# Optimization experiments

Hardware: AMD Instinct MI355X
Metric: run time of the kernel (lower is better)

The kernel has to match this reference:

```python
import jax, jax.numpy as jnp
import numpy as np

B, T, D, E, F, K = 1, 8192, 1024, 8, 4096, 2
CAP_FACTOR = 1.25
AUX_COEFF = 0.01


def setup_inputs() -> dict:
    key = jax.random.key(0)
    k0, k1, k2, k3, k4 = jax.random.split(key, 5)
    x = jax.random.normal(k0, (B, T, D), dtype=jnp.float32)
    Wr = jax.random.normal(k1, (E, D), dtype=jnp.float32) * 0.01  # router, std=0.01 per init
    s = 0.02
    Wg = jax.random.normal(k2, (E, F, D), dtype=jnp.float32) * s  # gate_proj per expert
    Wu = jax.random.normal(k3, (E, F, D), dtype=jnp.float32) * s  # up_proj per expert
    Wd = jax.random.normal(k4, (E, D, F), dtype=jnp.float32) * s  # down_proj per expert
    return {"x": x, "Wr": Wr, "Wg": Wg, "Wu": Wu, "Wd": Wd}


def reference(x, Wr, Wg, Wu, Wd):
    b, t, d = x.shape
    N = b * t
    capacity = max(int(t * K * CAP_FACTOR / E), 1)  # static, matches compute_capacity
    x_flat = x.reshape(N, d)

    # --- router ---
    logits = x_flat @ Wr.T                              # (N, E)
    probs = jax.nn.softmax(logits, axis=-1)
    topw_raw, topi = jax.lax.top_k(probs, K)            # (N, K)
    topw = topw_raw / (topw_raw.sum(-1, keepdims=True) + 1e-9)

    # --- dispatch order: slot-major (slot 0 over all tokens, then slot 1, ...) ---
    flat_e = topi.T.reshape(-1)                         # (K*N,) expert id per assignment
    flat_w = topw.T.reshape(-1)                         # (K*N,)
    tok = jnp.tile(jnp.arange(N), K)                    # (K*N,) token id per assignment

    oh = jax.nn.one_hot(flat_e, E, dtype=jnp.int32)     # (K*N, E)
    rank = (jnp.cumsum(oh, axis=0) - oh)[jnp.arange(K * N), flat_e]  # arrival rank per expert
    accepted = rank < capacity                          # dispatch_mask (slot-major flat)
    pos = jnp.where(accepted, rank, 0)
    dest = flat_e * capacity + pos                      # slot in flattened capacity buffer
    acc_f = accepted.astype(x.dtype)[:, None]

    # scatter tokens into capacity buffers (dropped tokens add zeros)
    buf = jnp.zeros((E * capacity, d), x.dtype).at[dest].add(x_flat[tok] * acc_f)
    expert_in = buf.reshape(E, capacity, d)

    # --- per-expert SwiGLU FFN (batched grouped GEMM) ---
    gate = jax.nn.silu(jnp.einsum('ecd,efd->ecf', expert_in, Wg))
    up = jnp.einsum('ecd,efd->ecf', expert_in, Wu)
    expert_out = jnp.einsum('ecf,edf->ecd', gate * up, Wd).reshape(E * capacity, d)

    # --- weighted combine back to token positions ---
    contrib = flat_w[:, None] * acc_f * expert_out[dest]
    out_flat = jnp.zeros((N, d), x.dtype).at[tok].add(contrib)
    output = out_flat.reshape(b, t, d)

    # --- load-balance aux loss ---
    counts = jnp.zeros(E, x.dtype).at[flat_e].add(accepted.astype(x.dtype))
    total = jnp.maximum(accepted.sum().astype(x.dtype), 1.0)
    f_i = counts / total
    P_i = probs.mean(0)
    aux_loss = AUX_COEFF * E * jnp.sum(f_i * P_i)
    return output, aux_loss
```

## Files before the change

### kernel.cpp

```cpp
#include <hip/hip_runtime.h>
#include <hip/hip_bf16.h>

#define N_TOK 8192
#define DIM   1024
#define NEXP  8
#define FF    4096
#define CAP   2560
#define NASSIGN (N_TOK * 2)

typedef __bf16 bf16;
typedef __bf16 bf16x8 __attribute__((ext_vector_type(8)));
typedef float  f32x4  __attribute__((ext_vector_type(4)));

__device__ __forceinline__ void gl2lds16(const bf16* g, bf16* l) {
    __builtin_amdgcn_global_load_lds(
        (const __attribute__((address_space(1))) unsigned int*)g,
        (__attribute__((address_space(3))) unsigned int*)l,
        16, 0, 0);
}

__global__ __launch_bounds__(256) void cvt_bf16_kernel(const float* __restrict__ in,
                                                       bf16* __restrict__ out, int n) {
    int stride = gridDim.x * blockDim.x * 8;
    for (int i = (blockIdx.x * blockDim.x + threadIdx.x) * 8; i < n; i += stride) {
        float4 a = *(const float4*)(in + i);
        float4 b = *(const float4*)(in + i + 4);
        bf16x8 o;
        o[0] = (bf16)a.x; o[1] = (bf16)a.y; o[2] = (bf16)a.z; o[3] = (bf16)a.w;
        o[4] = (bf16)b.x; o[5] = (bf16)b.y; o[6] = (bf16)b.z; o[7] = (bf16)b.w;
        *(bf16x8*)(out + i) = o;
    }
}

__global__ __launch_bounds__(256) void router_kernel(const float* __restrict__ x,
                                                     const float* __restrict__ Wr,
                                                     float* __restrict__ probs,
                                                     int* __restrict__ topi,
                                                     float* __restrict__ topw) {
    int wave = threadIdx.x >> 6;
    int lane = threadIdx.x & 63;
    int t = blockIdx.x * 4 + wave;
    const float* xr = x + (size_t)t * DIM;

    double acc[NEXP];
#pragma unroll
    for (int e = 0; e < NEXP; ++e) acc[e] = 0.0;
    for (int i = lane; i < DIM; i += 64) {
        double xv = (double)xr[i];
#pragma unroll
        for (int e = 0; e < NEXP; ++e) acc[e] += xv * (double)Wr[e * DIM + i];
    }
#pragma unroll
    for (int e = 0; e < NEXP; ++e) {
        double v = acc[e];
        for (int off = 32; off > 0; off >>= 1) v += __shfl_down(v, off, 64);
        acc[e] = v;
    }
    if (lane == 0) {
        double mx = acc[0];
        for (int e = 1; e < NEXP; ++e) if (acc[e] > mx) mx = acc[e];
        double p[NEXP], s = 0.0;
        for (int e = 0; e < NEXP; ++e) { p[e] = exp(acc[e] - mx); s += p[e]; }
        float pf[NEXP];
        for (int e = 0; e < NEXP; ++e) { pf[e] = (float)(p[e] / s); probs[t * NEXP + e] = pf[e]; }
        int e1 = 0;
        for (int e = 1; e < NEXP; ++e) if (acc[e] > acc[e1]) e1 = e;
        int e2 = -1;
        for (int e = 0; e < NEXP; ++e) {
            if (e == e1) continue;
            if (e2 < 0 || acc[e] > acc[e2]) e2 = e;
        }
        float w1 = pf[e1], w2 = pf[e2];
        float inv = 1.0f / (w1 + w2 + 1e-9f);
        topi[t * 2 + 0] = e1; topi[t * 2 + 1] = e2;
        topw[t * 2 + 0] = w1 * inv; topw[t * 2 + 1] = w2 * inv;
    }
}

__global__ __launch_bounds__(64) void rank_kernel(const int* __restrict__ topi,
                                                  int* __restrict__ dest,
                                                  int* __restrict__ accf,
                                                  int* __restrict__ counts) {
    int e = blockIdx.x;
    int lane = threadIdx.x;
    const int per = NASSIGN / 64;
    int base = lane * per;
    int cnt = 0;
    for (int i = 0; i < per; ++i) {
        int j = base + i;
        int t = j & (N_TOK - 1), s = j >> 13;
        if (topi[t * 2 + s] == e) cnt++;
    }
    int sum = cnt;
    for (int off = 1; off < 64; off <<= 1) {
        int v = __shfl_up(sum, off, 64);
        if (lane >= off) sum += v;
    }
    int r = sum - cnt;
    int total = __shfl(sum, 63, 64);
    for (int i = 0; i < per; ++i) {
        int j = base + i;
        int t = j & (N_TOK - 1), s = j >> 13;
        if (topi[t * 2 + s] == e) {
            int acc = (r < CAP) ? 1 : 0;
            dest[j] = e * CAP + (acc ? r : 0);
            accf[j] = acc;
            r++;
        }
    }
    if (lane == 63) counts[e] = (total < CAP) ? total : CAP;
}

__global__ __launch_bounds__(256) void gather_kernel(const float* __restrict__ x,
                                                     const int* __restrict__ dest,
                                                     const int* __restrict__ accf,
                                                     bf16* __restrict__ Xe) {
    int j = blockIdx.x;
    if (!accf[j]) return;
    int t = j & (N_TOK - 1);
    int d0 = threadIdx.x * 4;
    float4 v = *(const float4*)(x + (size_t)t * DIM + d0);
    union { bf16 h[4]; uint2 u; } tmp;
    tmp.h[0] = (bf16)v.x; tmp.h[1] = (bf16)v.y; tmp.h[2] = (bf16)v.z; tmp.h[3] = (bf16)v.w;
    *(uint2*)(Xe + (size_t)dest[j] * DIM + d0) = tmp.u;
}

__global__ __launch_bounds__(512, 2) void gateup_kernel(const bf16* __restrict__ Xe,
                                                        const bf16* __restrict__ Wg,
                                                        const bf16* __restrict__ Wu,
                                                        bf16* __restrict__ hbuf) {
    const int e = blockIdx.z;
    const int m0 = blockIdx.x * 256;
    const int n0 = blockIdx.y * 128;
    const int tid = threadIdx.x;
    const int lane = tid & 63;
    const int wave = tid >> 6;
    const int wr = wave >> 1;
    const int wc = wave & 1;
    const int r16 = lane & 15, c16 = lane >> 4;

    __shared__ bf16 As [2][256 * 64];
    __shared__ bf16 Bgs[2][128 * 64];
    __shared__ bf16 Bus[2][128 * 64];

    const int rsub = wave * 8 + (lane >> 3);
    const int csw  = ((lane & 7) ^ (lane >> 3)) * 8;
    const bf16* ga = Xe + (size_t)e * CAP * DIM + (size_t)(m0 + rsub) * DIM + csw;
    const bf16* gg = Wg + (size_t)e * FF * DIM + (size_t)(n0 + rsub) * DIM + csw;
    const bf16* gu = Wu + (size_t)e * FF * DIM + (size_t)(n0 + rsub) * DIM + csw;

    f32x4 accg[4][4] = {};
    f32x4 accu[4][4] = {};

    auto STAGE = [&](int kt) {
        const int b = kt & 1;
        const bf16* a = ga + kt * 64;
#pragma unroll
        for (int i = 0; i < 4; ++i)
            gl2lds16(a + (size_t)i * 64 * DIM, &As[b][(i * 64 + wave * 8) * 64]);
        const bf16* g = gg + kt * 64;
#pragma unroll
        for (int i = 0; i < 2; ++i)
            gl2lds16(g + (size_t)i * 64 * DIM, &Bgs[b][(i * 64 + wave * 8) * 64]);
        const bf16* u = gu + kt * 64;
#pragma unroll
        for (int i = 0; i < 2; ++i)
            gl2lds16(u + (size_t)i * 64 * DIM, &Bus[b][(i * 64 + wave * 8) * 64]);
    };

    STAGE(0);
    STAGE(1);

    for (int kt = 0; kt < DIM / 64; ++kt) {
        if (kt < DIM / 64 - 1) asm volatile("s_waitcnt vmcnt(8)" ::: "memory");
        else                   asm volatile("s_waitcnt vmcnt(0)" ::: "memory");
        __builtin_amdgcn_sched_barrier(0);
        __builtin_amdgcn_s_barrier();
        __builtin_amdgcn_sched_barrier(0);
        const int b = kt & 1;
#pragma unroll
        for (int kk = 0; kk < 2; ++kk) {
            bf16x8 a[4], bg[4], bu[4];
#pragma unroll
            for (int m = 0; m < 4; ++m) {
                int row = wr * 64 + m * 16 + r16;
                int phys = (kk * 4 + c16) ^ (row & 7);
                a[m] = *(const bf16x8*)&As[b][row * 64 + phys * 8];
            }
#pragma unroll
            for (int n = 0; n < 4; ++n) {
                int row = wc * 64 + n * 16 + r16;
                int phys = (kk * 4 + c16) ^ (row & 7);
                bg[n] = *(const bf16x8*)&Bgs[b][row * 64 + phys * 8];
            }
            __builtin_amdgcn_s_setprio(1);
#pragma unroll
            for (int m = 0; m < 4; ++m)
#pragma unroll
                for (int n = 0; n < 4; ++n)
                    accg[m][n] = __builtin_amdgcn_mfma_f32_16x16x32_bf16(a[m], bg[n], accg[m][n], 0, 0, 0);
            __builtin_amdgcn_s_setprio(0);
#pragma unroll
            for (int n = 0; n < 4; ++n) {
                int row = wc * 64 + n * 16 + r16;
                int phys = (kk * 4 + c16) ^ (row & 7);
                bu[n] = *(const bf16x8*)&Bus[b][row * 64 + phys * 8];
            }
            __builtin_amdgcn_s_setprio(1);
#pragma unroll
            for (int m = 0; m < 4; ++m)
#pragma unroll
                for (int n = 0; n < 4; ++n)
                    accu[m][n] = __builtin_amdgcn_mfma_f32_16x16x32_bf16(a[m], bu[n], accu[m][n], 0, 0, 0);
            __builtin_amdgcn_s_setprio(0);
        }
        __builtin_amdgcn_sched_barrier(0);
        __builtin_amdgcn_s_barrier();
        __builtin_amdgcn_sched_barrier(0);
        if (kt + 2 < DIM / 64) STAGE(kt + 2);
    }

    bf16* hp = hbuf + (size_t)e * CAP * FF;
#pragma unroll
    for (int m = 0; m < 4; ++m)
#pragma unroll
        for (int n = 0; n < 4; ++n)
#pragma unroll
            for (int j = 0; j < 4; ++j) {
                float g = accg[m][n][j];
                float u = accu[m][n][j];
                float h = (g / (1.f + __expf(-g))) * u;
                int gr = m0 + wr * 64 + m * 16 + c16 * 4 + j;
                int gc = n0 + wc * 64 + n * 16 + r16;
                hp[(size_t)gr * FF + gc] = (bf16)h;
            }
}

__global__ __launch_bounds__(256, 2) void down_kernel(const bf16* __restrict__ hbuf,
                                                      const bf16* __restrict__ Wd,
                                                      float* __restrict__ eo) {
    const int e = blockIdx.z;
    const int m0 = blockIdx.x * 128;
    const int n0 = blockIdx.y * 128;
    const int tid = threadIdx.x;
    const int lane = tid & 63;
    const int wave = tid >> 6;
    const int wr = wave >> 1;
    const int wc = wave & 1;
    const int r16 = lane & 15, c16 = lane >> 4;

    __shared__ bf16 As[2][128 * 64];
    __shared__ bf16 Bs[2][128 * 64];

    const int rsub = wave * 8 + (lane >> 3);
    const int csw  = ((lane & 7) ^ (lane >> 3)) * 8;
    const bf16* gaA = hbuf + (size_t)e * CAP * FF + (size_t)(m0 + rsub) * FF + csw;
    const bf16* gaB = Wd + (size_t)e * DIM * FF + (size_t)(n0 + rsub) * FF + csw;

    f32x4 acc[4][4] = {};

    auto STAGE = [&](int kt) {
        const int b = kt & 1;
        const bf16* a = gaA + kt * 64;
#pragma unroll
        for (int i = 0; i < 4; ++i)
            gl2lds16(a + (size_t)i * 32 * FF, &As[b][(i * 32 + wave * 8) * 64]);
        const bf16* w = gaB + kt * 64;
#pragma unroll
        for (int i = 0; i < 4; ++i)
            gl2lds16(w + (size_t)i * 32 * FF, &Bs[b][(i * 32 + wave * 8) * 64]);
    };

    STAGE(0);
    STAGE(1);

    for (int kt = 0; kt < FF / 64; ++kt) {
        if (kt < FF / 64 - 1) asm volatile("s_waitcnt vmcnt(8)" ::: "memory");
        else                  asm volatile("s_waitcnt vmcnt(0)" ::: "memory");
        __builtin_amdgcn_sched_barrier(0);
        __builtin_amdgcn_s_barrier();
        __builtin_amdgcn_sched_barrier(0);
        const int b = kt & 1;
#pragma unroll
        for (int kk = 0; kk < 2; ++kk) {
            bf16x8 a[4], w[4];
#pragma unroll
            for (int m = 0; m < 4; ++m) {
                int row = wr * 64 + m * 16 + r16;
                int phys = (kk * 4 + c16) ^ (row & 7);
                a[m] = *(const bf16x8*)&As[b][row * 64 + phys * 8];
            }
#pragma unroll
            for (int n = 0; n < 4; ++n) {
                int row = wc * 64 + n * 16 + r16;
                int phys = (kk * 4 + c16) ^ (row & 7);
                w[n] = *(const bf16x8*)&Bs[b][row * 64 + phys * 8];
            }
            __builtin_amdgcn_s_setprio(1);
#pragma unroll
            for (int m = 0; m < 4; ++m)
#pragma unroll
                for (int n = 0; n < 4; ++n)
                    acc[m][n] = __builtin_amdgcn_mfma_f32_16x16x32_bf16(a[m], w[n], acc[m][n], 0, 0, 0);
            __builtin_amdgcn_s_setprio(0);
        }
        __builtin_amdgcn_sched_barrier(0);
        __builtin_amdgcn_s_barrier();
        __builtin_amdgcn_sched_barrier(0);
        if (kt + 2 < FF / 64) STAGE(kt + 2);
    }

    float* op = eo + (size_t)e * CAP * DIM;
#pragma unroll
    for (int m = 0; m < 4; ++m)
#pragma unroll
        for (int n = 0; n < 4; ++n)
#pragma unroll
            for (int j = 0; j < 4; ++j) {
                int gr = m0 + wr * 64 + m * 16 + c16 * 4 + j;
                int gc = n0 + wc * 64 + n * 16 + r16;
                op[(size_t)gr * DIM + gc] = acc[m][n][j];
            }
}

__global__ __launch_bounds__(256) void combine_kernel(const float* __restrict__ eo,
                                                      const int* __restrict__ dest,
                                                      const int* __restrict__ accf,
                                                      const float* __restrict__ topw,
                                                      float* __restrict__ out) {
    int t = blockIdx.x;
    float w0 = accf[t] ? topw[t * 2 + 0] : 0.f;
    float w1 = accf[N_TOK + t] ? topw[t * 2 + 1] : 0.f;
    const float* r0 = eo + (size_t)dest[t] * DIM;
    const float* r1 = eo + (size_t)dest[N_TOK + t] * DIM;
    int d = threadIdx.x * 4;
    float4 a = *(const float4*)(r0 + d);
    float4 b = *(const float4*)(r1 + d);
    float4 o;
    o.x = w0 * a.x + w1 * b.x;
    o.y = w0 * a.y + w1 * b.y;
    o.z = w0 * a.z + w1 * b.z;
    o.w = w0 * a.w + w1 * b.w;
    *(float4*)(out + (size_t)t * DIM + d) = o;
}

__global__ __launch_bounds__(256) void aux_kernel(const float* __restrict__ probs,
                                                  const int* __restrict__ counts,
                                                  float* __restrict__ out_aux) {
    __shared__ float sm[256][NEXP];
    float loc[NEXP];
#pragma unroll
    for (int e = 0; e < NEXP; ++e) loc[e] = 0.f;
    for (int t = threadIdx.x; t < N_TOK; t += 256)
#pragma unroll
        for (int e = 0; e < NEXP; ++e) loc[e] += probs[t * NEXP + e];
#pragma unroll
    for (int e = 0; e < NEXP; ++e) sm[threadIdx.x][e] = loc[e];
    __syncthreads();
    for (int s = 128; s > 0; s >>= 1) {
        if (threadIdx.x < s)
#pragma unroll
            for (int e = 0; e < NEXP; ++e) sm[threadIdx.x][e] += sm[threadIdx.x + s][e];
        __syncthreads();
    }
    if (threadIdx.x == 0) {
        int tot = 0;
        for (int e = 0; e < NEXP; ++e) tot += counts[e];
        float totf = tot > 0 ? (float)tot : 1.f;
        float aux = 0.f;
        for (int e = 0; e < NEXP; ++e)
            aux += ((float)counts[e] / totf) * (sm[0][e] / (float)N_TOK);
        out_aux[0] = 0.01f * (float)NEXP * aux;
    }
}

extern "C" void kernel_launch(void* const* d_in, const int* in_sizes, int n_in,
                              void* d_out, int out_size, void* d_ws, size_t ws_size,
                              hipStream_t stream) {
    const float* x  = (const float*)d_in[0];
    const float* Wr = (const float*)d_in[1];
    const float* Wg = (const float*)d_in[2];
    const float* Wu = (const float*)d_in[3];
    const float* Wd = (const float*)d_in[4];
    float* out = (float*)d_out;

    char* ws = (char*)d_ws;
    size_t off = 0;
    auto alloc = [&](size_t bytes) -> void* {
        void* p = ws + off;
        off += (bytes + 255) & ~(size_t)255;
        return p;
    };
    const size_t NW = (size_t)NEXP * FF * DIM;
    bf16*  Wg_bf = (bf16*)alloc(NW * sizeof(bf16));
    bf16*  Wu_bf = (bf16*)alloc(NW * sizeof(bf16));
    bf16*  Wd_bf = (bf16*)alloc(NW * sizeof(bf16));
    bf16*  Xe    = (bf16*)alloc((size_t)NEXP * CAP * DIM * sizeof(bf16));
    bf16*  hbuf  = (bf16*)alloc((size_t)NEXP * CAP * FF * sizeof(bf16));
    float* eo    = (float*)alloc((size_t)NEXP * CAP * DIM * sizeof(float));
    float* probs = (float*)alloc((size_t)N_TOK * NEXP * sizeof(float));
    int*   topi  = (int*)alloc((size_t)N_TOK * 2 * sizeof(int));
    float* topw  = (float*)alloc((size_t)N_TOK * 2 * sizeof(float));
    int*   dst   = (int*)alloc((size_t)NASSIGN * sizeof(int));
    int*   accf  = (int*)alloc((size_t)NASSIGN * sizeof(int));
    int*   cnts  = (int*)alloc(NEXP * sizeof(int));

    cvt_bf16_kernel<<<2048, 256, 0, stream>>>(Wg, Wg_bf, (int)NW);
    cvt_bf16_kernel<<<2048, 256, 0, stream>>>(Wu, Wu_bf, (int)NW);
    cvt_bf16_kernel<<<2048, 256, 0, stream>>>(Wd, Wd_bf, (int)NW);
    router_kernel<<<N_TOK / 4, 256, 0, stream>>>(x, Wr, probs, topi, topw);
    rank_kernel<<<NEXP, 64, 0, stream>>>(topi, dst, accf, cnts);
    gather_kernel<<<NASSIGN, 256, 0, stream>>>(x, dst, accf, Xe);
    gateup_kernel<<<dim3(CAP / 256, FF / 128, NEXP), 512, 0, stream>>>(Xe, Wg_bf, Wu_bf, hbuf);
    down_kernel<<<dim3(CAP / 128, DIM / 128, NEXP), 256, 0, stream>>>(hbuf, Wd_bf, eo);
    combine_kernel<<<N_TOK, 256, 0, stream>>>(eo, dst, accf, topw, out);
    aux_kernel<<<1, 256, 0, stream>>>(probs, cnts, out + (size_t)N_TOK * DIM);
}
```

Measured before the change: 912.3 us.

## Share a 256x256 four-phase GEMM core; split-K down projection with bf16 partials

Adds a shared 256x256-tile GEMM core that splits each k-step into four phases of LDS reads and MFMAs separated by barriers. The gate/up kernel now interleaves gate and up rows into one 256-row B tile so both products share the A fragments. The down projection moves to 256x256 tiles with split-K over two halves of FF, and writes its partial sums as bf16, which combine adds together. This aims for more MFMA work per byte loaded and enough blocks to fill the GPU, at the cost of lower precision in the down-projection output and more barriers.

```diff
diff --git a/kernel.cpp b/kernel.cpp
--- a/kernel.cpp
+++ b/kernel.cpp
@@ -10,6 +10,7 @@
 
 typedef __bf16 bf16;
 typedef __bf16 bf16x8 __attribute__((ext_vector_type(8)));
+typedef __bf16 bf16x4v __attribute__((ext_vector_type(4)));
 typedef float  f32x4  __attribute__((ext_vector_type(4)));
 
 __device__ __forceinline__ void gl2lds16(const bf16* g, bf16* l) {
@@ -17,6 +18,97 @@
         (const __attribute__((address_space(1))) unsigned int*)g,
         (__attribute__((address_space(3))) unsigned int*)l,
         16, 0, 0);
+}
+
+template <int NT>
+__device__ __forceinline__ void gemm256_core(
+    const bf16* __restrict__ gA, size_t astep,
+    const bf16* __restrict__ gB, size_t bstep,
+    bf16* As, bf16* Bs, f32x4 acc[8][4], int wave, int lane)
+{
+    const int wm = wave >> 2, wn = wave & 3;
+    const int r16 = lane & 15, c16 = lane >> 4;
+
+    auto STAGE = [&](int kt) {
+        const int b = kt & 1;
+        const bf16* a  = gA + kt * 64;
+        const bf16* bb = gB + kt * 64;
+#pragma unroll
+        for (int g = 0; g < 4; ++g)
+            gl2lds16(a + (size_t)g * astep, &As[b * (256 * 64) + (g * 64 + wave * 8) * 64]);
+#pragma unroll
+        for (int g = 0; g < 4; ++g)
+            gl2lds16(bb + (size_t)g * bstep, &Bs[b * (256 * 64) + (g * 64 + wave * 8) * 64]);
+    };
+
+    STAGE(0);
+    STAGE(1);
+
+    bf16x8 af[4][2], bfr[2][2];
+
+    for (int kt = 0; kt < NT; ++kt) {
+        if (kt < NT - 1) asm volatile("s_waitcnt vmcnt(8)" ::: "memory");
+        else             asm volatile("s_waitcnt vmcnt(0)" ::: "memory");
+        __builtin_amdgcn_sched_barrier(0);
+        __builtin_amdgcn_s_barrier();
+        __builtin_amdgcn_sched_barrier(0);
+        const bf16* Asb = &As[(kt & 1) * (256 * 64)];
+        const bf16* Bsb = &Bs[(kt & 1) * (256 * 64)];
+
+#define DS_A(mh)                                                          \
+        _Pragma("unroll")                                                 \
+        for (int m = 0; m < 4; ++m) {                                     \
+            _Pragma("unroll")                                             \
+            for (int kk = 0; kk < 2; ++kk) {                              \
+                int row = wm * 128 + (mh) * 64 + m * 16 + r16;            \
+                int phys = (kk * 4 + c16) ^ (row & 7);                    \
+                af[m][kk] = *(const bf16x8*)&Asb[row * 64 + phys * 8];    \
+            } }
+#define DS_B(nh)                                                          \
+        _Pragma("unroll")                                                 \
+        for (int n = 0; n < 2; ++n) {                                     \
+            _Pragma("unroll")                                             \
+            for (int kk = 0; kk < 2; ++kk) {                              \
+                int row = wn * 64 + ((nh) * 2 + n) * 16 + r16;            \
+                int phys = (kk * 4 + c16) ^ (row & 7);                    \
+                bfr[n][kk] = *(const bf16x8*)&Bsb[row * 64 + phys * 8];   \
+            } }
+#define PH_IN                                                             \
+        __builtin_amdgcn_sched_barrier(0);                                \
+        __builtin_amdgcn_s_barrier();                                     \
+        asm volatile("s_waitcnt lgkmcnt(0)" ::: "memory");                \
+        __builtin_amdgcn_sched_barrier(0);
+#define PH_MFMA(mh, nh)                                                   \
+        __builtin_amdgcn_s_setprio(1);                                    \
+        _Pragma("unroll")                                                 \
+        for (int m = 0; m < 4; ++m)                                       \
+            _Pragma("unroll")                                             \
+            for (int n = 0; n < 2; ++n)                                   \
+                _Pragma("unroll")                                         \
+                for (int kk = 0; kk < 2; ++kk)                            \
+                    acc[(mh) * 4 + m][(nh) * 2 + n] =                     \
+                        __builtin_amdgcn_mfma_f32_16x16x32_bf16(          \
+                            af[m][kk], bfr[n][kk],                        \
+                            acc[(mh) * 4 + m][(nh) * 2 + n], 0, 0, 0);    \
+        __builtin_amdgcn_s_setprio(0);
+#define PH_OUT                                                            \
+        __builtin_amdgcn_sched_barrier(0);                                \
+        __builtin_amdgcn_s_barrier();                                     \
+        __builtin_amdgcn_sched_barrier(0);
+
+        DS_A(0) DS_B(0) PH_IN PH_MFMA(0, 0) PH_OUT
+        DS_B(1)         PH_IN PH_MFMA(0, 1) PH_OUT
+        DS_A(1) DS_B(0) PH_IN PH_MFMA(1, 0) PH_OUT
+        DS_B(1)         PH_IN PH_MFMA(1, 1) PH_OUT
+
+#undef DS_A
+#undef DS_B
+#undef PH_IN
+#undef PH_MFMA
+#undef PH_OUT
+
+        if (kt + 2 < NT) STAGE(kt + 2);
+    }
 }
 
 __global__ __launch_bounds__(256) void cvt_bf16_kernel(const float* __restrict__ in,
@@ -131,199 +223,76 @@
                                                         bf16* __restrict__ hbuf) {
     const int e = blockIdx.z;
     const int m0 = blockIdx.x * 256;
-    const int n0 = blockIdx.y * 128;
-    const int tid = threadIdx.x;
-    const int lane = tid & 63;
-    const int wave = tid >> 6;
-    const int wr = wave >> 1;
-    const int wc = wave & 1;
+    const int n0f = blockIdx.y * 128;
+    const int tid = threadIdx.x, lane = tid & 63, wave = tid >> 6;
+    const int wm = wave >> 2, wn = wave & 3;
     const int r16 = lane & 15, c16 = lane >> 4;
 
-    __shared__ bf16 As [2][256 * 64];
-    __shared__ bf16 Bgs[2][128 * 64];
-    __shared__ bf16 Bus[2][128 * 64];
+    __shared__ bf16 As[2 * 256 * 64];
+    __shared__ bf16 Bs[2 * 256 * 64];
 
     const int rsub = wave * 8 + (lane >> 3);
     const int csw  = ((lane & 7) ^ (lane >> 3)) * 8;
-    const bf16* ga = Xe + (size_t)e * CAP * DIM + (size_t)(m0 + rsub) * DIM + csw;
-    const bf16* gg = Wg + (size_t)e * FF * DIM + (size_t)(n0 + rsub) * DIM + csw;
-    const bf16* gu = Wu + (size_t)e * FF * DIM + (size_t)(n0 + rsub) * DIM + csw;
-
-    f32x4 accg[4][4] = {};
-    f32x4 accu[4][4] = {};
-
-    auto STAGE = [&](int kt) {
-        const int b = kt & 1;
-        const bf16* a = ga + kt * 64;
-#pragma unroll
-        for (int i = 0; i < 4; ++i)
-            gl2lds16(a + (size_t)i * 64 * DIM, &As[b][(i * 64 + wave * 8) * 64]);
-        const bf16* g = gg + kt * 64;
-#pragma unroll
-        for (int i = 0; i < 2; ++i)
-            gl2lds16(g + (size_t)i * 64 * DIM, &Bgs[b][(i * 64 + wave * 8) * 64]);
-        const bf16* u = gu + kt * 64;
-#pragma unroll
-        for (int i = 0; i < 2; ++i)
-            gl2lds16(u + (size_t)i * 64 * DIM, &Bus[b][(i * 64 + wave * 8) * 64]);
-    };
-
-    STAGE(0);
-    STAGE(1);
-
-    for (int kt = 0; kt < DIM / 64; ++kt) {
-        if (kt < DIM / 64 - 1) asm volatile("s_waitcnt vmcnt(8)" ::: "memory");
-        else                   asm volatile("s_waitcnt vmcnt(0)" ::: "memory");
-        __builtin_amdgcn_sched_barrier(0);
-        __builtin_amdgcn_s_barrier();
-        __builtin_amdgcn_sched_barrier(0);
-        const int b = kt & 1;
-#pragma unroll
-        for (int kk = 0; kk < 2; ++kk) {
-            bf16x8 a[4], bg[4], bu[4];
-#pragma unroll
-            for (int m = 0; m < 4; ++m) {
-                int row = wr * 64 + m * 16 + r16;
-                int phys = (kk * 4 + c16) ^ (row & 7);
-                a[m] = *(const bf16x8*)&As[b][row * 64 + phys * 8];
-            }
-#pragma unroll
-            for (int n = 0; n < 4; ++n) {
-                int row = wc * 64 + n * 16 + r16;
-                int phys = (kk * 4 + c16) ^ (row & 7);
-                bg[n] = *(const bf16x8*)&Bgs[b][row * 64 + phys * 8];
-            }
-            __builtin_amdgcn_s_setprio(1);
-#pragma unroll
-            for (int m = 0; m < 4; ++m)
-#pragma unroll
-                for (int n = 0; n < 4; ++n)
-                    accg[m][n] = __builtin_amdgcn_mfma_f32_16x16x32_bf16(a[m], bg[n], accg[m][n], 0, 0, 0);
-            __builtin_amdgcn_s_setprio(0);
-#pragma unroll
-            for (int n = 0; n < 4; ++n) {
-                int row = wc * 64 + n * 16 + r16;
-                int phys = (kk * 4 + c16) ^ (row & 7);
-                bu[n] = *(const bf16x8*)&Bus[b][row * 64 + phys * 8];
-            }
-            __builtin_amdgcn_s_setprio(1);
-#pragma unroll
-            for (int m = 0; m < 4; ++m)
-#pragma unroll
-                for (int n = 0; n < 4; ++n)
-                    accu[m][n] = __builtin_amdgcn_mfma_f32_16x16x32_bf16(a[m], bu[n], accu[m][n], 0, 0, 0);
-            __builtin_amdgcn_s_setprio(0);
-        }
-        __builtin_amdgcn_sched_barrier(0);
-        __builtin_amdgcn_s_barrier();
-        __builtin_amdgcn_sched_barrier(0);
-        if (kt + 2 < DIM / 64) STAGE(kt + 2);
-    }
+    const bf16* gA = Xe + (size_t)e * CAP * DIM + (size_t)(m0 + rsub) * DIM + csw;
+    const int bff = n0f + ((rsub >> 5) & 1) * 16 + (rsub & 15);
+    const bf16* gB = (((rsub >> 4) & 1) ? Wu : Wg)
+                   + (size_t)e * FF * DIM + (size_t)bff * DIM + csw;
+
+    f32x4 acc[8][4] = {};
+    gemm256_core<DIM / 64>(gA, (size_t)64 * DIM, gB, (size_t)32 * DIM, As, Bs, acc, wave, lane);
 
     bf16* hp = hbuf + (size_t)e * CAP * FF;
 #pragma unroll
-    for (int m = 0; m < 4; ++m)
-#pragma unroll
-        for (int n = 0; n < 4; ++n)
+    for (int m = 0; m < 8; ++m)
+#pragma unroll
+        for (int np = 0; np < 2; ++np)
 #pragma unroll
             for (int j = 0; j < 4; ++j) {
-                float g = accg[m][n][j];
-                float u = accu[m][n][j];
+                float g = acc[m][2 * np + 0][j];
+                float u = acc[m][2 * np + 1][j];
                 float h = (g / (1.f + __expf(-g))) * u;
-                int gr = m0 + wr * 64 + m * 16 + c16 * 4 + j;
-                int gc = n0 + wc * 64 + n * 16 + r16;
+                int gr = m0 + wm * 128 + m * 16 + c16 * 4 + j;
+                int gc = n0f + wn * 32 + np * 16 + r16;
                 hp[(size_t)gr * FF + gc] = (bf16)h;
             }
 }
 
-__global__ __launch_bounds__(256, 2) void down_kernel(const bf16* __restrict__ hbuf,
+__global__ __launch_bounds__(512, 2) void down_kernel(const bf16* __restrict__ hbuf,
                                                       const bf16* __restrict__ Wd,
-                                                      float* __restrict__ eo) {
-    const int e = blockIdx.z;
-    const int m0 = blockIdx.x * 128;
-    const int n0 = blockIdx.y * 128;
-    const int tid = threadIdx.x;
-    const int lane = tid & 63;
-    const int wave = tid >> 6;
-    const int wr = wave >> 1;
-    const int wc = wave & 1;
+                                                      bf16* __restrict__ eo) {
+    const int e  = blockIdx.z >> 1;
+    const int kh = blockIdx.z & 1;
+    const int m0 = blockIdx.x * 256;
+    const int n0 = blockIdx.y * 256;
+    const int tid = threadIdx.x, lane = tid & 63, wave = tid >> 6;
+    const int wm = wave >> 2, wn = wave & 3;
     const int r16 = lane & 15, c16 = lane >> 4;
 
-    __shared__ bf16 As[2][128 * 64];
-    __shared__ bf16 Bs[2][128 * 64];
+    __shared__ bf16 As[2 * 256 * 64];
+    __shared__ bf16 Bs[2 * 256 * 64];
 
     const int rsub = wave * 8 + (lane >> 3);
     const int csw  = ((lane & 7) ^ (lane >> 3)) * 8;
-    const bf16* gaA = hbuf + (size_t)e * CAP * FF + (size_t)(m0 + rsub) * FF + csw;
-    const bf16* gaB = Wd + (size_t)e * DIM * FF + (size_t)(n0 + rsub) * FF + csw;
-
-    f32x4 acc[4][4] = {};
-
-    auto STAGE = [&](int kt) {
-        const int b = kt & 1;
-        const bf16* a = gaA + kt * 64;
-#pragma unroll
-        for (int i = 0; i < 4; ++i)
-            gl2lds16(a + (size_t)i * 32 * FF, &As[b][(i * 32 + wave * 8) * 64]);
-        const bf16* w = gaB + kt * 64;
-#pragma unroll
-        for (int i = 0; i < 4; ++i)
-            gl2lds16(w + (size_t)i * 32 * FF, &Bs[b][(i * 32 + wave * 8) * 64]);
-    };
-
-    STAGE(0);
-    STAGE(1);
-
-    for (int kt = 0; kt < FF / 64; ++kt) {
-        if (kt < FF / 64 - 1) asm volatile("s_waitcnt vmcnt(8)" ::: "memory");
-        else                  asm volatile("s_waitcnt vmcnt(0)" ::: "memory");
-        __builtin_amdgcn_sched_barrier(0);
-        __builtin_amdgcn_s_barrier();
-        __builtin_amdgcn_sched_barrier(0);
-        const int b = kt & 1;
-#pragma unroll
-        for (int kk = 0; kk < 2; ++kk) {
-            bf16x8 a[4], w[4];
-#pragma unroll
-            for (int m = 0; m < 4; ++m) {
-                int row = wr * 64 + m * 16 + r16;
-                int phys = (kk * 4 + c16) ^ (row & 7);
-                a[m] = *(const bf16x8*)&As[b][row * 64 + phys * 8];
+    const bf16* gA = hbuf + (size_t)e * CAP * FF + (size_t)(m0 + rsub) * FF + kh * (FF / 2) + csw;
+    const bf16* gB = Wd + (size_t)e * DIM * FF + (size_t)(n0 + rsub) * FF + kh * (FF / 2) + csw;
+
+    f32x4 acc[8][4] = {};
+    gemm256_core<FF / 128>(gA, (size_t)64 * FF, gB, (size_t)64 * FF, As, Bs, acc, wave, lane);
+
+    bf16* op = eo + (size_t)kh * NEXP * CAP * DIM + (size_t)e * CAP * DIM;
+#pragma unroll
+    for (int m = 0; m < 8; ++m)
+#pragma unroll
+        for (int n = 0; n < 4; ++n)
+#pragma unroll
+            for (int j = 0; j < 4; ++j) {
+                int gr = m0 + wm * 128 + m * 16 + c16 * 4 + j;
+                int gc = n0 + wn * 64 + n * 16 + r16;
+                op[(size_t)gr * DIM + gc] = (bf16)acc[m][n][j];
             }
-#pragma unroll
-            for (int n = 0; n < 4; ++n) {
-                int row = wc * 64 + n * 16 + r16;
-                int phys = (kk * 4 + c16) ^ (row & 7);
-                w[n] = *(const bf16x8*)&Bs[b][row * 64 + phys * 8];
-            }
-            __builtin_amdgcn_s_setprio(1);
-#pragma unroll
-            for (int m = 0; m < 4; ++m)
-#pragma unroll
-                for (int n = 0; n < 4; ++n)
-                    acc[m][n] = __builtin_amdgcn_mfma_f32_16x16x32_bf16(a[m], w[n], acc[m][n], 0, 0, 0);
-            __builtin_amdgcn_s_setprio(0);
-        }
-        __builtin_amdgcn_sched_barrier(0);
-        __builtin_amdgcn_s_barrier();
-        __builtin_amdgcn_sched_barrier(0);
-        if (kt + 2 < FF / 64) STAGE(kt + 2);
-    }
-
-    float* op = eo + (size_t)e * CAP * DIM;
-#pragma unroll
-    for (int m = 0; m < 4; ++m)
-#pragma unroll
-        for (int n = 0; n < 4; ++n)
-#pragma unroll
-            for (int j = 0; j < 4; ++j) {
-                int gr = m0 + wr * 64 + m * 16 + c16 * 4 + j;
-                int gc = n0 + wc * 64 + n * 16 + r16;
-                op[(size_t)gr * DIM + gc] = acc[m][n][j];
-            }
-}
-
-__global__ __launch_bounds__(256) void combine_kernel(const float* __restrict__ eo,
+}
+
+__global__ __launch_bounds__(256) void combine_kernel(const bf16* __restrict__ eo,
                                                       const int* __restrict__ dest,
                                                       const int* __restrict__ accf,
                                                       const float* __restrict__ topw,
@@ -331,16 +300,19 @@
     int t = blockIdx.x;
     float w0 = accf[t] ? topw[t * 2 + 0] : 0.f;
     float w1 = accf[N_TOK + t] ? topw[t * 2 + 1] : 0.f;
-    const float* r0 = eo + (size_t)dest[t] * DIM;
-    const float* r1 = eo + (size_t)dest[N_TOK + t] * DIM;
+    size_t off1 = (size_t)NEXP * CAP * DIM;
+    const bf16* a0 = eo + (size_t)dest[t] * DIM;
+    const bf16* b0 = eo + (size_t)dest[N_TOK + t] * DIM;
     int d = threadIdx.x * 4;
-    float4 a = *(const float4*)(r0 + d);
-    float4 b = *(const float4*)(r1 + d);
+    bf16x4v a00 = *(const bf16x4v*)(a0 + d);
+    bf16x4v a01 = *(const bf16x4v*)(a0 + off1 + d);
+    bf16x4v b00 = *(const bf16x4v*)(b0 + d);
+    bf16x4v b01 = *(const bf16x4v*)(b0 + off1 + d);
     float4 o;
-    o.x = w0 * a.x + w1 * b.x;
-    o.y = w0 * a.y + w1 * b.y;
-    o.z = w0 * a.z + w1 * b.z;
-    o.w = w0 * a.w + w1 * b.w;
+    o.x = w0 * ((float)a00[0] + (float)a01[0]) + w1 * ((float)b00[0] + (float)b01[0]);
+    o.y = w0 * ((float)a00[1] + (float)a01[1]) + w1 * ((float)b00[1] + (float)b01[1]);
+    o.z = w0 * ((float)a00[2] + (float)a01[2]) + w1 * ((float)b00[2] + (float)b01[2]);
+    o.w = w0 * ((float)a00[3] + (float)a01[3]) + w1 * ((float)b00[3] + (float)b01[3]);
     *(float4*)(out + (size_t)t * DIM + d) = o;
 }
 
@@ -397,7 +369,7 @@
     bf16*  Wd_bf = (bf16*)alloc(NW * sizeof(bf16));
     bf16*  Xe    = (bf16*)alloc((size_t)NEXP * CAP * DIM * sizeof(bf16));
     bf16*  hbuf  = (bf16*)alloc((size_t)NEXP * CAP * FF * sizeof(bf16));
-    float* eo    = (float*)alloc((size_t)NEXP * CAP * DIM * sizeof(float));
+    bf16*  eo    = (bf16*)alloc((size_t)2 * NEXP * CAP * DIM * sizeof(bf16));
     float* probs = (float*)alloc((size_t)N_TOK * NEXP * sizeof(float));
     int*   topi  = (int*)alloc((size_t)N_TOK * 2 * sizeof(int));
     float* topw  = (float*)alloc((size_t)N_TOK * 2 * sizeof(float));
@@ -412,7 +384,7 @@
     rank_kernel<<<NEXP, 64, 0, stream>>>(topi, dst, accf, cnts);
     gather_kernel<<<NASSIGN, 256, 0, stream>>>(x, dst, accf, Xe);
     gateup_kernel<<<dim3(CAP / 256, FF / 128, NEXP), 512, 0, stream>>>(Xe, Wg_bf, Wu_bf, hbuf);
-    down_kernel<<<dim3(CAP / 128, DIM / 128, NEXP), 256, 0, stream>>>(hbuf, Wd_bf, eo);
+    down_kernel<<<dim3(CAP / 256, DIM / 256, NEXP * 2), 512, 0, stream>>>(hbuf, Wd_bf, eo);
     combine_kernel<<<N_TOK, 256, 0, stream>>>(eo, dst, accf, topw, out);
     aux_kernel<<<1, 256, 0, stream>>>(probs, cnts, out + (size_t)N_TOK * DIM);
 }
```

New measurement: 1.024 ms. 1.12x slower.
